# Performance work log

Hardware: AMD Instinct MI355X
Metric: run time of the kernel (lower is better)

## Reference

```python
import jax, jax.numpy as jnp
import numpy as np

SIGMA = 25.0
EPS = 1e-5
TWO_PI = 2.0 * np.pi


def _gn(x, gamma, beta, groups):
    # GroupNorm over (C//G, H, W) per group, per-channel affine.
    B, C, H, W = x.shape
    xg = x.reshape(B, groups, -1)
    m = xg.mean(-1, keepdims=True)
    v = xg.var(-1, keepdims=True)
    xn = ((xg - m) * jax.lax.rsqrt(v + EPS)).reshape(B, C, H, W)
    return xn * gamma[None, :, None, None] + beta[None, :, None, None]


def _conv3(x, k, b):
    y = jax.lax.conv_general_dilated(x, k, (1, 1), 'SAME',
                                     dimension_numbers=('NCHW', 'OIHW', 'NCHW'))
    return y + b[None, :, None, None]


def _tconv2(x, k, b):
    # ConvTranspose2d kernel=2 stride=2 (no overlap) == einsum + reshape.
    # k: [C_in, C_out, 2, 2]
    B, C, H, W = x.shape
    O = k.shape[1]
    y = jnp.einsum('bchw,codq->bohdwq', x, k).reshape(B, O, 2 * H, 2 * W)
    return y + b[None, :, None, None]


def _conv1(x, k, b):
    # 1x1 conv; k: [C_out, C_in]
    return jnp.einsum('bchw,oc->bohw', x, k) + b[None, :, None, None]


def _pool(x):
    B, C, H, W = x.shape
    return x.reshape(B, C, H // 2, 2, W // 2, 2).max(axis=(3, 5))


def _std(t):
    return jnp.sqrt((SIGMA ** (2.0 * t) - 1.0) / (2.0 * jnp.log(SIGMA)))


def setup_inputs() -> dict:
    key = jax.random.key(0)
    ks = jax.random.split(key, 16)
    B, H, W = 64, 128, 128
    E = 2 * W  # 256 = embed_dim

    def w(k, shape, fan_in):
        return jax.random.normal(k, shape, jnp.float32) / np.sqrt(fan_in)

    inp = {
        'x': jax.random.normal(ks[0], (B, 1, H, W), jnp.float32),
        't': jax.random.uniform(ks[1], (B,), jnp.float32, 1e-3, 1.0),
        'Wf': jax.random.normal(ks[2], (H, W), jnp.float32) * 30.0,  # fixed Fourier features
        'fc1_w': w(ks[3], (E, E), E),
        'fc1_b': jnp.zeros((E,), jnp.float32),
        'conv1_k': w(ks[4], (6, 1, 3, 3), 9),
        'conv1_b': jnp.zeros((6,), jnp.float32),
        'gn1_g': jnp.ones((6,), jnp.float32), 'gn1_b': jnp.zeros((6,), jnp.float32),
        'conv2_k': w(ks[5], (24, 6, 3, 3), 6 * 9),
        'conv2_b': jnp.zeros((24,), jnp.float32),
        'gn2_g': jnp.ones((24,), jnp.float32), 'gn2_b': jnp.zeros((24,), jnp.float32),
        't3_k': w(ks[6], (24, 24, 2, 2), 24 * 4),
        't3_b': jnp.zeros((24,), jnp.float32),
        'gn3_g': jnp.ones((48,), jnp.float32), 'gn3_b': jnp.zeros((48,), jnp.float32),
        't4_k': w(ks[7], (48, 12, 2, 2), 48 * 4),
        't4_b': jnp.zeros((12,), jnp.float32),
        'gn4_g': jnp.ones((18,), jnp.float32), 'gn4_b': jnp.zeros((18,), jnp.float32),
        't5_k': w(ks[8], (6, 18), 18),
        't5_b': jnp.zeros((6,), jnp.float32),
        'gn5_g': jnp.ones((6,), jnp.float32), 'gn5_b': jnp.zeros((6,), jnp.float32),
        'fin_k': w(ks[9], (1, 6), 6),
        'fin_b': jnp.zeros((1,), jnp.float32),
    }
    return inp


def reference(x, t, Wf, fc1_w, fc1_b, conv1_k, conv1_b, gn1_g, gn1_b,
              conv2_k, conv2_b, gn2_g, gn2_b, t3_k, t3_b, gn3_g, gn3_b,
              t4_k, t4_b, gn4_g, gn4_b, t5_k, t5_b, gn5_g, gn5_b,
              fin_k, fin_b):
    # Vectorized Gaussian Fourier projection: [B,1,H,W] -> [B,1,H,2W]
    p = x * Wf[None, None] * TWO_PI
    xe = jnp.concatenate([jnp.sin(p), jnp.cos(p)], axis=-1)
    # fc1 on last dim (embed_dim = 2W)
    xf = jnp.einsum('bchw,ow->bcho', xe, fc1_w) + fc1_b
    c1 = _conv3(xf, conv1_k, conv1_b)                              # [B,6,H,2W]
    p1 = _pool(jax.nn.relu(_gn(c1, gn1_g, gn1_b, 6)))              # [B,6,H/2,W]
    c2 = _conv3(p1, conv2_k, conv2_b)                              # [B,24,H/2,W]
    p2 = _pool(jax.nn.relu(_gn(c2, gn2_g, gn2_b, 24)))             # [B,24,H/4,W/2]
    a = p2 * jax.nn.sigmoid(p2)                                    # SiLU bottleneck
    u3 = _tconv2(a, t3_k, t3_b)                                    # [B,24,H/2,W]
    g3 = _gn(jnp.concatenate([c2, u3], axis=1), gn3_g, gn3_b, 6)   # 48 ch
    u4 = _tconv2(g3, t4_k, t4_b)                                   # [B,12,H,2W]
    g4 = _gn(jnp.concatenate([c1, u4], axis=1), gn4_g, gn4_b, 6)   # 18 ch
    u5 = _conv1(g4, t5_k, t5_b)                                    # [B,6,H,2W]
    g5 = _gn(u5, gn5_g, gn5_b, 6)
    return _conv1(g5, fin_k, fin_b) / _std(t)[:, None, None, None]
```

## Files before the change

### kernel.cpp

```cpp
#include <hip/hip_runtime.h>
#include <hip/hip_bf16.h>
#include <math.h>

#define BB 64
#define HH 128
#define WW 128
#define EE 256
#define HP (HH*EE)
#define H2 64
#define W2 128
#define PL2 (H2*W2)
#define H4 32
#define W4 64
#define PL4 (H4*W4)

typedef __hip_bfloat16 bf;
typedef unsigned short ushortt;
typedef __attribute__((ext_vector_type(8))) __bf16 b8v;
typedef __attribute__((ext_vector_type(4))) float f4v;

__device__ __forceinline__ float tof(bf v)    { return __bfloat162float(v); }
__device__ __forceinline__ bf    tob(float v) { return __float2bfloat16(v); }
__device__ __forceinline__ unsigned int bfbits(float v) {
    return (unsigned int)__builtin_bit_cast(ushortt, __float2bfloat16(v));
}
__device__ __forceinline__ float b2f(unsigned int u16) {
    unsigned int x = u16 << 16;
    return __builtin_bit_cast(float, x);
}
__device__ __forceinline__ void wred2(float& s, float& q) {
    #pragma unroll
    for (int m = 32; m; m >>= 1) {
        s += __shfl_xor(s, m);
        q += __shfl_xor(q, m);
    }
}
__device__ __forceinline__ void wred2_32(float& s, float& q) {
    #pragma unroll
    for (int m = 16; m; m >>= 1) {
        s += __shfl_xor(s, m);
        q += __shfl_xor(q, m);
    }
}

__global__ __launch_bounds__(256) void k_fourier_fc1(
    const float* __restrict__ x, const float* __restrict__ Wf,
    const float* __restrict__ fc1_w, const float* __restrict__ fc1_b,
    bf* __restrict__ xf, float* __restrict__ mb)
{
    __shared__ ushortt sA[64*264];
    __shared__ ushortt sB[64*264];
    int t = threadIdx.x;
    for (int i = blockIdx.x*256 + t; i < 9216; i += 512*256) mb[i] = 0.f;
    int rb = blockIdx.x >> 2, cb = blockIdx.x & 3;
    int row0 = rb*64, col0 = cb*64;
    const float TP = 6.2831853071795864769f;
    for (int it = 0; it < 32; ++it) {
        int i = it*256 + t;
        int r = i >> 7, w = i & 127;
        int rg = row0 + r;
        float p = x[(size_t)rg*WW + w] * Wf[(size_t)(rg & (HH-1))*WW + w] * TP;
        sA[r*264 + w]       = (ushortt)bfbits(__sinf(p));
        sA[r*264 + 128 + w] = (ushortt)bfbits(__cosf(p));
    }
    #pragma unroll
    for (int it = 0; it < 16; ++it) {
        int i = it*256 + t;
        int o = i >> 6, c4 = i & 63;
        float4 w4 = *(const float4*)(fc1_w + (size_t)(col0 + o)*EE + c4*4);
        uint2 pk;
        pk.x = bfbits(w4.x) | (bfbits(w4.y) << 16);
        pk.y = bfbits(w4.z) | (bfbits(w4.w) << 16);
        *(uint2*)&sB[o*264 + c4*4] = pk;
    }
    __syncthreads();
    int lane = t & 63, wid = t >> 6;
    int m = lane & 15, kq = (lane >> 4) * 8;
    f4v acc[4] = {};
    const ushortt* aBase = &sA[(wid*16 + m)*264 + kq];
    #pragma unroll
    for (int k0 = 0; k0 < 8; ++k0) {
        b8v av = *(const b8v*)(aBase + k0*32);
        #pragma unroll
        for (int t4 = 0; t4 < 4; ++t4) {
            b8v bv = *(const b8v*)&sB[(t4*16 + m)*264 + k0*32 + kq];
            acc[t4] = __builtin_amdgcn_mfma_f32_16x16x32_bf16(av, bv, acc[t4], 0, 0, 0);
        }
    }
    int rbase = row0 + wid*16 + (lane >> 4)*4;
    #pragma unroll
    for (int t4 = 0; t4 < 4; ++t4) {
        int col = col0 + t4*16 + m;
        float bias = fc1_b[col];
        #pragma unroll
        for (int r = 0; r < 4; ++r)
            xf[(size_t)(rbase + r)*EE + col] = tob(acc[t4][r] + bias);
    }
}

__global__ __launch_bounds__(256) void k_conv1(
    const bf* __restrict__ xf, const float* __restrict__ k,
    const float* __restrict__ bias, bf* __restrict__ c1, float* __restrict__ mc1)
{
    __shared__ ushortt sT[6*272];
    __shared__ float red[4][6][2];
    int t = threadIdx.x;
    int ht = blockIdx.x & 31, b = blockIdx.x >> 5;
    int h0 = ht*4;
    const bf* src = xf + (size_t)b*HP;
    if (t < 192) {
        int r = t >> 5, i = t & 31;
        int gy = h0 - 1 + r;
        uint4 v = {0,0,0,0};
        if (gy >= 0 && gy < HH) v = *(const uint4*)(src + (size_t)gy*EE + i*8);
        *(uint4*)&sT[r*272 + 8 + i*8] = v;
    } else if (t < 204) {
        int e = t - 192;
        int r = e >> 1, s = e & 1;
        uint4 z = {0,0,0,0};
        *(uint4*)&sT[r*272 + s*264] = z;
    }
    __syncthreads();
    int wq = (t & 63)*4, hl = t >> 6;
    int lane = t & 63, wid = t >> 6;
    float v[3][6];
    #pragma unroll
    for (int ky = 0; ky < 3; ++ky)
      #pragma unroll
      for (int j = 0; j < 6; ++j)
        v[ky][j] = b2f((unsigned)sT[(hl+ky)*272 + 7 + wq + j]);
    int h = h0 + hl;
    #pragma unroll
    for (int o = 0; o < 6; ++o) {
        float bv = bias[o];
        float a0=bv, a1=bv, a2=bv, a3=bv;
        #pragma unroll
        for (int ky = 0; ky < 3; ++ky)
          #pragma unroll
          for (int kx = 0; kx < 3; ++kx) {
            float wv = k[o*9 + ky*3 + kx];
            a0 += v[ky][kx+0]*wv;
            a1 += v[ky][kx+1]*wv;
            a2 += v[ky][kx+2]*wv;
            a3 += v[ky][kx+3]*wv;
          }
        uint2 pk;
        pk.x = bfbits(a0) | (bfbits(a1) << 16);
        pk.y = bfbits(a2) | (bfbits(a3) << 16);
        *(uint2*)(c1 + ((size_t)(b*6+o)*HH + h)*EE + wq) = pk;
        float s = a0+a1+a2+a3, q = a0*a0+a1*a1+a2*a2+a3*a3;
        wred2(s, q);
        if (lane == 0) { red[wid][o][0] = s; red[wid][o][1] = q; }
    }
    __syncthreads();
    if (t < 6) {
        float S = 0.f, Q = 0.f;
        #pragma unroll
        for (int wv = 0; wv < 4; ++wv) { S += red[wv][t][0]; Q += red[wv][t][1]; }
        atomicAdd(&mc1[((size_t)b*6 + t)*2],     S);
        atomicAdd(&mc1[((size_t)b*6 + t)*2 + 1], Q);
    }
}

__global__ __launch_bounds__(256) void k_conv2(
    const bf* __restrict__ c1, const float* __restrict__ mc1,
    const float* __restrict__ g1, const float* __restrict__ be1,
    const float* __restrict__ kw, const float* __restrict__ bias,
    bf* __restrict__ c2, float* __restrict__ mc2)
{
    __shared__ ushortt sA[256*72];
    __shared__ ushortt sW[32*72];
    __shared__ ushortt sP[6*4*136];
    __shared__ float ssl[12];
    __shared__ float redS[24], redQ[24];
    int t = threadIdx.x;
    int ht = blockIdx.x & 31, b = blockIdx.x >> 5;
    int h0 = ht*2;
    int lane = t & 63, wid = t >> 6;
    if (t < 24) { redS[t] = 0.f; redQ[t] = 0.f; }
    if (t < 6) {
        float s = mc1[((size_t)b*6 + t)*2], q = mc1[((size_t)b*6 + t)*2 + 1];
        float mean = s * (1.f/HP);
        float var  = q * (1.f/HP) - mean*mean;
        float rstd = rsqrtf(var + 1e-5f);
        float sc = g1[t]*rstd;
        ssl[t*2] = sc; ssl[t*2+1] = be1[t] - mean*sc;
    }
    for (int i = t; i < 1152; i += 256) ((unsigned*)sW)[i] = 0;
    __syncthreads();
    for (int i = t; i < 3120; i += 256) {
        int c = i / 520, rem = i % 520;
        int ry = rem / 130, rx = rem % 130;
        int gy = h0 - 1 + ry, gx = rx - 1;
        float v = 0.f;
        if (gy >= 0 && gy < H2 && gx >= 0 && gx < W2) {
            const bf* pp = c1 + ((size_t)(b*6+c)*HH + 2*gy)*EE + 2*gx;
            unsigned r0 = *(const unsigned*)pp;
            unsigned r1 = *(const unsigned*)(pp + EE);
            float sc = ssl[c*2], sh = ssl[c*2+1];
            float e0 = fmaxf(b2f(r0 & 0xffff)*sc+sh, 0.f);
            float e1 = fmaxf(b2f(r0 >> 16)   *sc+sh, 0.f);
            float e2 = fmaxf(b2f(r1 & 0xffff)*sc+sh, 0.f);
            float e3 = fmaxf(b2f(r1 >> 16)   *sc+sh, 0.f);
            v = fmaxf(fmaxf(e0,e1), fmaxf(e2,e3));
        }
        sP[c*544 + ry*136 + rx] = (ushortt)bfbits(v);
    }
    for (int e = t; e < 1296; e += 256) {
        int o = e / 54, kk = e % 54;
        sW[o*72 + kk] = (ushortt)bfbits(kw[e]);
    }
    __syncthreads();
    {
        int r = t >> 7, xx = t & 127;
        unsigned u[32];
        #pragma unroll
        for (int p = 0; p < 27; ++p) {
            int k0 = 2*p, k1 = 2*p + 1;
            int c0 = k0/9, y0 = (k0%9)/3, x0 = k0%3;
            int c1i = k1/9, y1 = (k1%9)/3, x1 = k1%3;
            unsigned lo = sP[c0*544 + (r+y0)*136 + xx + x0];
            unsigned hi = sP[c1i*544 + (r+y1)*136 + xx + x1];
            u[p] = lo | (hi << 16);
        }
        #pragma unroll
        for (int p = 27; p < 32; ++p) u[p] = 0;
        #pragma unroll
        for (int e = 0; e < 8; ++e) {
            uint4 pk; pk.x = u[4*e]; pk.y = u[4*e+1]; pk.z = u[4*e+2]; pk.w = u[4*e+3];
            *(uint4*)&sA[t*72 + e*8] = pk;
        }
    }
    __syncthreads();
    int m = lane & 15, kq = (lane >> 4)*8;
    b8v wv[2][2];
    #pragma unroll
    for (int nt = 0; nt < 2; ++nt)
      #pragma unroll
      for (int ks = 0; ks < 2; ++ks)
        wv[nt][ks] = *(const b8v*)&sW[(nt*16 + m)*72 + ks*32 + kq];
    f4v acc[4][2] = {};
    #pragma unroll
    for (int mt = 0; mt < 4; ++mt) {
        const ushortt* ab = &sA[(wid*64 + mt*16 + m)*72 + kq];
        b8v a0 = *(const b8v*)(ab);
        b8v a1 = *(const b8v*)(ab + 32);
        #pragma unroll
        for (int nt = 0; nt < 2; ++nt) {
            acc[mt][nt] = __builtin_amdgcn_mfma_f32_16x16x32_bf16(a0, wv[nt][0], acc[mt][nt], 0, 0, 0);
            acc[mt][nt] = __builtin_amdgcn_mfma_f32_16x16x32_bf16(a1, wv[nt][1], acc[mt][nt], 0, 0, 0);
        }
    }
    __syncthreads();
    ushortt* sC = sA;
    int q4 = lane >> 4;
    #pragma unroll
    for (int mt = 0; mt < 4; ++mt) {
        int pxb = wid*64 + mt*16 + q4*4;
        #pragma unroll
        for (int nt = 0; nt < 2; ++nt) {
            int o = nt*16 + m;
            if (o < 24) {
                float bo = bias[o];
                #pragma unroll
                for (int r = 0; r < 4; ++r) {
                    int px = pxb + r;
                    sC[o*272 + (px >> 7)*136 + (px & 127)] =
                        (ushortt)bfbits(acc[mt][nt][r] + bo);
                }
            }
        }
    }
    __syncthreads();
    #pragma unroll
    for (int j = 0; j < 3; ++j) {
        int idx = j*256 + t;
        int o = idx >> 5;
        int rem = idx & 31;
        int r = rem >> 4, x8 = (rem & 15)*8;
        uint4 v = *(const uint4*)&sC[o*272 + r*136 + x8];
        *(uint4*)(c2 + ((size_t)(b*24+o)*H2 + h0 + r)*W2 + x8) = v;
        float v0 = b2f(v.x & 0xffff), v1 = b2f(v.x >> 16);
        float v2 = b2f(v.y & 0xffff), v3 = b2f(v.y >> 16);
        float v4 = b2f(v.z & 0xffff), v5 = b2f(v.z >> 16);
        float v6 = b2f(v.w & 0xffff), v7 = b2f(v.w >> 16);
        float s = v0+v1+v2+v3+v4+v5+v6+v7;
        float qv = v0*v0+v1*v1+v2*v2+v3*v3+v4*v4+v5*v5+v6*v6+v7*v7;
        wred2_32(s, qv);
        if ((lane & 31) == 0) { atomicAdd(&redS[o], s); atomicAdd(&redQ[o], qv); }
    }
    __syncthreads();
    if (t < 24) {
        atomicAdd(&mc2[((size_t)b*24 + t)*2],     redS[t]);
        atomicAdd(&mc2[((size_t)b*24 + t)*2 + 1], redQ[t]);
    }
}

__global__ __launch_bounds__(256) void k_tconv3(
    const bf* __restrict__ c2, const float* __restrict__ mc2,
    const float* __restrict__ g2, const float* __restrict__ be2,
    const float* __restrict__ k3, const float* __restrict__ b3,
    bf* __restrict__ u3, float* __restrict__ mu3)
{
    __shared__ ushortt sBuf[27648];
    __shared__ float redS[24], redQ[24];
    __shared__ float ssl[48];
    ushortt* sA = sBuf;
    ushortt* sW = sBuf + 10240;
    int t = threadIdx.x;
    int b = blockIdx.x >> 3, pg = blockIdx.x & 7;
    int lane = t & 63, wid = t >> 6;
    if (t < 24) {
        redS[t] = 0.f; redQ[t] = 0.f;
        float s = mc2[((size_t)b*24 + t)*2], q = mc2[((size_t)b*24 + t)*2 + 1];
        float mean = s * (1.f/PL2);
        float var  = q * (1.f/PL2) - mean*mean;
        float rstd = rsqrtf(var + 1e-5f);
        float sc = g2[t]*rstd;
        ssl[t*2] = sc; ssl[t*2+1] = be2[t] - mean*sc;
    }
    #pragma unroll
    for (int j = 0; j < 9; ++j) {
        int e = j*256 + t;
        int c = e / 96, n = e % 96;
        sW[n*40 + c] = (ushortt)bfbits(k3[e]);
    }
    if (t < 96) { uint4 z = {0,0,0,0}; *(uint4*)&sW[t*40 + 24] = z; }
    { uint4 z = {0,0,0,0}; *(uint4*)&sA[t*40 + 24] = z; }
    __syncthreads();
    #pragma unroll
    for (int j = 0; j < 12; ++j) {
        int i = j*256 + t;
        int c = i >> 7, pr = i & 127;
        int px0 = pr*2;
        int h4 = (pg*256 + px0) >> 6, w4 = px0 & 63;
        const bf* pp = c2 + ((size_t)b*24 + c)*PL2 + (size_t)(2*h4)*W2 + 2*w4;
        uint2 r0 = *(const uint2*)pp;
        uint2 r1 = *(const uint2*)(pp + W2);
        float sc = ssl[c*2], sh = ssl[c*2+1];
        float e0 = fmaxf(b2f(r0.x & 0xffff)*sc+sh, 0.f);
        float e1 = fmaxf(b2f(r0.x >> 16)   *sc+sh, 0.f);
        float f0 = fmaxf(b2f(r1.x & 0xffff)*sc+sh, 0.f);
        float f1 = fmaxf(b2f(r1.x >> 16)   *sc+sh, 0.f);
        float m0 = fmaxf(fmaxf(e0,e1), fmaxf(f0,f1));
        m0 = m0 / (1.f + expf(-m0));
        float e2 = fmaxf(b2f(r0.y & 0xffff)*sc+sh, 0.f);
        float e3 = fmaxf(b2f(r0.y >> 16)   *sc+sh, 0.f);
        float f2 = fmaxf(b2f(r1.y & 0xffff)*sc+sh, 0.f);
        float f3 = fmaxf(b2f(r1.y >> 16)   *sc+sh, 0.f);
        float m1 = fmaxf(fmaxf(e2,e3), fmaxf(f2,f3));
        m1 = m1 / (1.f + expf(-m1));
        sA[px0*40 + c]     = (ushortt)bfbits(m0);
        sA[(px0+1)*40 + c] = (ushortt)bfbits(m1);
    }
    __syncthreads();
    int m = lane & 15, kq = (lane >> 4)*8;
    b8v wv[6];
    #pragma unroll
    for (int nt = 0; nt < 6; ++nt)
        wv[nt] = *(const b8v*)&sW[(nt*16 + m)*40 + kq];
    f4v acc[4][6] = {};
    #pragma unroll
    for (int mt = 0; mt < 4; ++mt) {
        b8v av = *(const b8v*)&sA[(wid*64 + mt*16 + m)*40 + kq];
        #pragma unroll
        for (int nt = 0; nt < 6; ++nt)
            acc[mt][nt] = __builtin_amdgcn_mfma_f32_16x16x32_bf16(av, wv[nt], acc[mt][nt], 0, 0, 0);
    }
    __syncthreads();
    ushortt* sC = sBuf;
    int q4 = lane >> 4;
    #pragma unroll
    for (int mt = 0; mt < 4; ++mt) {
        int pxb = wid*64 + mt*16 + q4*4;
        #pragma unroll
        for (int nt = 0; nt < 6; ++nt) {
            int n = nt*16 + m;
            int o = n >> 2, d = (n >> 1) & 1, qq = n & 1;
            float bo = b3[o];
            #pragma unroll
            for (int r = 0; r < 4; ++r) {
                int px = pxb + r;
                int yl = ((px >> 6) << 1) + d;
                int xx = ((px & 63) << 1) + qq;
                sC[o*1152 + yl*144 + xx] = (ushortt)bfbits(acc[mt][nt][r] + bo);
            }
        }
    }
    __syncthreads();
    bf* outb = u3 + (size_t)b*24*PL2;
    #pragma unroll
    for (int j = 0; j < 12; ++j) {
        int idx = j*256 + t;
        int o = idx >> 7;
        int rem = idx & 127;
        int yl = rem >> 4, xc = (rem & 15)*8;
        uint4 v = *(const uint4*)&sC[o*1152 + yl*144 + xc];
        *(uint4*)(outb + ((size_t)o*H2 + pg*8 + yl)*W2 + xc) = v;
        float v0 = b2f(v.x & 0xffff), v1 = b2f(v.x >> 16);
        float v2 = b2f(v.y & 0xffff), v3 = b2f(v.y >> 16);
        float v4 = b2f(v.z & 0xffff), v5 = b2f(v.z >> 16);
        float v6 = b2f(v.w & 0xffff), v7 = b2f(v.w >> 16);
        float s = v0+v1+v2+v3+v4+v5+v6+v7;
        float qv = v0*v0+v1*v1+v2*v2+v3*v3+v4*v4+v5*v5+v6*v6+v7*v7;
        wred2(s, qv);
        if (lane == 0) { atomicAdd(&redS[o], s); atomicAdd(&redQ[o], qv); }
    }
    __syncthreads();
    if (t < 24) {
        atomicAdd(&mu3[((size_t)b*24 + t)*2],     redS[t]);
        atomicAdd(&mu3[((size_t)b*24 + t)*2 + 1], redQ[t]);
    }
}

__global__ __launch_bounds__(256) void k_tconv4(
    const bf* __restrict__ c2, const bf* __restrict__ u3,
    const float* __restrict__ mc2, const float* __restrict__ mu3,
    const float* __restrict__ g3, const float* __restrict__ be3,
    const float* __restrict__ k4, const float* __restrict__ bias4,
    bf* __restrict__ u4, float* __restrict__ mu4)
{
    __shared__ ushortt sA[256*64];
    __shared__ ushortt sW[48*64];
    __shared__ float redS[12], redQ[12];
    __shared__ float ssl[96];
    int t = threadIdx.x;
    int b = blockIdx.x >> 5, pg = blockIdx.x & 31;
    int lane = t & 63, wid = t >> 6;
    int m = lane & 15, q4 = lane >> 4;
    if (t < 12) { redS[t] = 0.f; redQ[t] = 0.f; }
    if (t < 6) {
        float s = 0.f, q = 0.f;
        #pragma unroll
        for (int cl = 0; cl < 8; ++cl) {
            int gc = t*8 + cl;
            const float* p = (gc < 24) ? mc2 + ((size_t)b*24 + gc)*2
                                       : mu3 + ((size_t)b*24 + gc - 24)*2;
            s += p[0]; q += p[1];
        }
        float inv_n = 1.f/((float)PL2*8.f);
        float mean = s*inv_n;
        float var  = q*inv_n - mean*mean;
        float rstd = rsqrtf(var + 1e-5f);
        #pragma unroll
        for (int cl = 0; cl < 8; ++cl) {
            int gc = t*8 + cl;
            float sc = g3[gc]*rstd;
            ssl[gc*2] = sc; ssl[gc*2+1] = be3[gc] - mean*sc;
        }
    }
    #pragma unroll
    for (int j = 0; j < 9; ++j) {
        int e = j*256 + t;
        int c = e / 48, n = e % 48;
        sW[n*64 + ((((c >> 3) ^ (n & 7)) << 3) | (c & 7))] = (ushortt)bfbits(k4[e]);
    }
    if (t < 96) {
        uint4 z = {0,0,0,0};
        int n = t >> 1, kb = 6 + (t & 1);
        *(uint4*)&sW[n*64 + ((kb ^ (n & 7)) << 3)] = z;
    }
    {
        int px = t;
        int pix = pg*256 + px;
        const bf* c2p = c2 + (size_t)b*24*PL2 + pix;
        const bf* u3p = u3 + (size_t)b*24*PL2 + pix;
        #pragma unroll
        for (int g = 0; g < 6; ++g) {
            unsigned pr[4];
            #pragma unroll
            for (int hc = 0; hc < 4; ++hc) {
                int c0 = g*8 + hc*2;
                float r0 = (c0 < 24) ? tof(c2p[(size_t)c0*PL2]) : tof(u3p[(size_t)(c0-24)*PL2]);
                float r1 = (c0+1 < 24) ? tof(c2p[(size_t)(c0+1)*PL2]) : tof(u3p[(size_t)(c0+1-24)*PL2]);
                float v0 = r0 * ssl[2*c0]   + ssl[2*c0+1];
                float v1 = r1 * ssl[2*c0+2] + ssl[2*c0+3];
                pr[hc] = bfbits(v0) | (bfbits(v1) << 16);
            }
            uint4 pk; pk.x = pr[0]; pk.y = pr[1]; pk.z = pr[2]; pk.w = pr[3];
            *(uint4*)&sA[px*64 + ((g ^ (px & 7)) << 3)] = pk;
        }
        uint4 z = {0,0,0,0};
        *(uint4*)&sA[px*64 + ((6 ^ (px & 7)) << 3)] = z;
        *(uint4*)&sA[px*64 + ((7 ^ (px & 7)) << 3)] = z;
    }
    __syncthreads();
    b8v bfr[3][2];
    #pragma unroll
    for (int nt = 0; nt < 3; ++nt) {
        int n = nt*16 + m;
        #pragma unroll
        for (int ks = 0; ks < 2; ++ks)
            bfr[nt][ks] = *(const b8v*)&sW[n*64 + (((ks*4 + q4) ^ (n & 7)) << 3)];
    }
    f4v acc[4][3] = {};
    #pragma unroll
    for (int mt = 0; mt < 4; ++mt) {
        int px = wid*64 + mt*16 + m;
        b8v a0 = *(const b8v*)&sA[px*64 + (((q4)     ^ (px & 7)) << 3)];
        b8v a1 = *(const b8v*)&sA[px*64 + (((4 + q4) ^ (px & 7)) << 3)];
        #pragma unroll
        for (int nt = 0; nt < 3; ++nt) {
            acc[mt][nt] = __builtin_amdgcn_mfma_f32_16x16x32_bf16(a0, bfr[nt][0], acc[mt][nt], 0, 0, 0);
            acc[mt][nt] = __builtin_amdgcn_mfma_f32_16x16x32_bf16(a1, bfr[nt][1], acc[mt][nt], 0, 0, 0);
        }
    }
    float sAcc[3] = {0.f, 0.f, 0.f}, qAcc[3] = {0.f, 0.f, 0.f};
    int qq = m & 1;
    #pragma unroll
    for (int nt = 0; nt < 3; ++nt) {
        int n = nt*16 + m;
        int o = n >> 2, d = (n >> 1) & 1;
        float bo = bias4[o];
        #pragma unroll
        for (int mt = 0; mt < 4; ++mt) {
            int pxb = wid*64 + mt*16 + q4*4;
            unsigned wds[4];
            float s = 0.f, q = 0.f;
            #pragma unroll
            for (int r = 0; r < 4; ++r) {
                float v = acc[mt][nt][r] + bo;
                float vp = __shfl_xor(v, 1);
                unsigned lo = bfbits(v), hi = bfbits(vp);
                wds[r] = lo | (hi << 16);
                float f0 = b2f(lo), f1 = b2f(hi);
                s += f0 + f1;
                q += f0*f0 + f1*f1;
            }
            if (qq == 0) {
                int h2 = (pg*256 + pxb) >> 7;
                int w0 = pxb & 127;
                uint4 pk; pk.x = wds[0]; pk.y = wds[1]; pk.z = wds[2]; pk.w = wds[3];
                *(uint4*)(u4 + (((size_t)(b*12 + o))*HH + 2*h2 + d)*EE + 2*w0) = pk;
                sAcc[nt] += s; qAcc[nt] += q;
            }
        }
    }
    #pragma unroll
    for (int nt = 0; nt < 3; ++nt) {
        float s = sAcc[nt], q = qAcc[nt];
        s += __shfl_xor(s, 2);  q += __shfl_xor(q, 2);
        s += __shfl_xor(s, 16); q += __shfl_xor(q, 16);
        s += __shfl_xor(s, 32); q += __shfl_xor(q, 32);
        if ((lane & 51) == 0) {
            int o = nt*4 + (m >> 2);
            atomicAdd(&redS[o], s);
            atomicAdd(&redQ[o], q);
        }
    }
    __syncthreads();
    if (t < 12) {
        atomicAdd(&mu4[((size_t)b*12 + t)*2],     redS[t]);
        atomicAdd(&mu4[((size_t)b*12 + t)*2 + 1], redQ[t]);
    }
}

__global__ __launch_bounds__(256) void k_conv1x1_u5(
    const bf* __restrict__ c1, const bf* __restrict__ u4,
    const float* __restrict__ mc1, const float* __restrict__ mu4,
    const float* __restrict__ g4, const float* __restrict__ be4,
    const float* __restrict__ k, const float* __restrict__ bias,
    bf* __restrict__ u5, float* __restrict__ mu5)
{
    __shared__ float red[4][6][2];
    __shared__ float ssl[36];
    int t = threadIdx.x;
    int b  = blockIdx.x >> 4;
    int pg = blockIdx.x & 15;
    int pix = pg*2048 + t*8;
    int lane = t & 63, wid = t >> 6;
    if (t < 6) {
        float s = 0.f, q = 0.f;
        #pragma unroll
        for (int cl = 0; cl < 3; ++cl) {
            int gc = t*3 + cl;
            const float* p = (gc < 6) ? mc1 + ((size_t)b*6 + gc)*2
                                      : mu4 + ((size_t)b*12 + gc - 6)*2;
            s += p[0]; q += p[1];
        }
        float inv_n = 1.f/((float)HP*3.f);
        float mean = s*inv_n;
        float var  = q*inv_n - mean*mean;
        float rstd = rsqrtf(var + 1e-5f);
        #pragma unroll
        for (int cl = 0; cl < 3; ++cl) {
            int gc = t*3 + cl;
            float sc = g4[gc]*rstd;
            ssl[gc*2] = sc; ssl[gc*2+1] = be4[gc] - mean*sc;
        }
    }
    __syncthreads();
    const bf* c1p = c1 + ((size_t)b*6)*HP + pix;
    const bf* u4p = u4 + ((size_t)b*12)*HP + pix;
    float acc[6][8];
    #pragma unroll
    for (int o = 0; o < 6; ++o) {
        float bv = bias[o];
        #pragma unroll
        for (int j = 0; j < 8; ++j) acc[o][j] = bv;
    }
    #pragma unroll
    for (int c = 0; c < 18; ++c) {
        uint4 r = (c < 6) ? *(const uint4*)(c1p + (size_t)c*HP)
                          : *(const uint4*)(u4p + (size_t)(c-6)*HP);
        float sc = ssl[2*c], sh = ssl[2*c+1];
        float v[8];
        v[0] = b2f(r.x & 0xffff)*sc + sh;  v[1] = b2f(r.x >> 16)*sc + sh;
        v[2] = b2f(r.y & 0xffff)*sc + sh;  v[3] = b2f(r.y >> 16)*sc + sh;
        v[4] = b2f(r.z & 0xffff)*sc + sh;  v[5] = b2f(r.z >> 16)*sc + sh;
        v[6] = b2f(r.w & 0xffff)*sc + sh;  v[7] = b2f(r.w >> 16)*sc + sh;
        #pragma unroll
        for (int o = 0; o < 6; ++o) {
            float wv = k[o*18 + c];
            #pragma unroll
            for (int j = 0; j < 8; ++j) acc[o][j] += v[j]*wv;
        }
    }
    #pragma unroll
    for (int o = 0; o < 6; ++o) {
        uint4 pk;
        pk.x = bfbits(acc[o][0]) | (bfbits(acc[o][1]) << 16);
        pk.y = bfbits(acc[o][2]) | (bfbits(acc[o][3]) << 16);
        pk.z = bfbits(acc[o][4]) | (bfbits(acc[o][5]) << 16);
        pk.w = bfbits(acc[o][6]) | (bfbits(acc[o][7]) << 16);
        *(uint4*)(u5 + ((size_t)(b*6+o))*HP + pix) = pk;
        float s = 0.f, q = 0.f;
        #pragma unroll
        for (int j = 0; j < 8; ++j) { s += acc[o][j]; q += acc[o][j]*acc[o][j]; }
        wred2(s, q);
        if (lane == 0) { red[wid][o][0] = s; red[wid][o][1] = q; }
    }
    __syncthreads();
    if (t < 6) {
        float S = 0.f, Q = 0.f;
        #pragma unroll
        for (int wv = 0; wv < 4; ++wv) { S += red[wv][t][0]; Q += red[wv][t][1]; }
        atomicAdd(&mu5[((size_t)b*6 + t)*2],     S);
        atomicAdd(&mu5[((size_t)b*6 + t)*2 + 1], Q);
    }
}

__global__ __launch_bounds__(256) void k_final(
    const bf* __restrict__ u5, const float* __restrict__ mu5,
    const float* __restrict__ g5, const float* __restrict__ be5,
    const float* __restrict__ k, const float* __restrict__ bias,
    const float* __restrict__ t, float* __restrict__ out)
{
    __shared__ float ssl[12];
    int tt = threadIdx.x;
    int b = blockIdx.x >> 4;
    int pix = ((blockIdx.x & 15)*256 + tt)*8;
    if (tt < 6) {
        float s = mu5[((size_t)b*6 + tt)*2], q = mu5[((size_t)b*6 + tt)*2 + 1];
        float mean = s * (1.f/HP);
        float var  = q * (1.f/HP) - mean*mean;
        float rstd = rsqrtf(var + 1e-5f);
        float sc = g5[tt]*rstd;
        ssl[tt*2] = sc; ssl[tt*2+1] = be5[tt] - mean*sc;
    }
    __syncthreads();
    const bf* up = u5 + (size_t)b*6*HP + pix;
    float bv = bias[0];
    float a[8];
    #pragma unroll
    for (int j = 0; j < 8; ++j) a[j] = bv;
    #pragma unroll
    for (int c = 0; c < 6; ++c) {
        uint4 r = *(const uint4*)(up + (size_t)c*HP);
        float sc = ssl[2*c], sh = ssl[2*c+1];
        float wv = k[c];
        a[0] += (b2f(r.x & 0xffff)*sc + sh) * wv;
        a[1] += (b2f(r.x >> 16)   *sc + sh) * wv;
        a[2] += (b2f(r.y & 0xffff)*sc + sh) * wv;
        a[3] += (b2f(r.y >> 16)   *sc + sh) * wv;
        a[4] += (b2f(r.z & 0xffff)*sc + sh) * wv;
        a[5] += (b2f(r.z >> 16)   *sc + sh) * wv;
        a[6] += (b2f(r.w & 0xffff)*sc + sh) * wv;
        a[7] += (b2f(r.w >> 16)   *sc + sh) * wv;
    }
    float tb = t[b];
    const float lns = 3.2188758248682007492f;
    float var = (expf(2.f*tb*lns) - 1.f) / (2.f*lns);
    float rs = rsqrtf(var);
    float4 o0; o0.x = a[0]*rs; o0.y = a[1]*rs; o0.z = a[2]*rs; o0.w = a[3]*rs;
    float4 o1; o1.x = a[4]*rs; o1.y = a[5]*rs; o1.z = a[6]*rs; o1.w = a[7]*rs;
    float* op = out + (size_t)b*HP + pix;
    *(float4*)op       = o0;
    *(float4*)(op + 4) = o1;
}

extern "C" void kernel_launch(void* const* d_in, const int* in_sizes, int n_in,
                              void* d_out, int out_size, void* d_ws, size_t ws_size,
                              hipStream_t stream)
{
    const float* x       = (const float*)d_in[0];
    const float* t       = (const float*)d_in[1];
    const float* Wf      = (const float*)d_in[2];
    const float* fc1_w   = (const float*)d_in[3];
    const float* fc1_b   = (const float*)d_in[4];
    const float* conv1_k = (const float*)d_in[5];
    const float* conv1_b = (const float*)d_in[6];
    const float* gn1_g   = (const float*)d_in[7];
    const float* gn1_b   = (const float*)d_in[8];
    const float* conv2_k = (const float*)d_in[9];
    const float* conv2_b = (const float*)d_in[10];
    const float* gn2_g   = (const float*)d_in[11];
    const float* gn2_b   = (const float*)d_in[12];
    const float* t3_k    = (const float*)d_in[13];
    const float* t3_b    = (const float*)d_in[14];
    const float* gn3_g   = (const float*)d_in[15];
    const float* gn3_b   = (const float*)d_in[16];
    const float* t4_k    = (const float*)d_in[17];
    const float* t4_b    = (const float*)d_in[18];
    const float* gn4_g   = (const float*)d_in[19];
    const float* gn4_b   = (const float*)d_in[20];
    const float* t5_k    = (const float*)d_in[21];
    const float* t5_b    = (const float*)d_in[22];
    const float* gn5_g   = (const float*)d_in[23];
    const float* gn5_b   = (const float*)d_in[24];
    const float* fin_k   = (const float*)d_in[25];
    const float* fin_b   = (const float*)d_in[26];

    bf* wsb = (bf*)d_ws;
    bf* c1 = wsb;
    bf* c2 = wsb + 12582912;
    bf* u3 = wsb + 25165824;
    bf* u4 = wsb + 37748736;
    bf* xf = wsb + 39845888;
    bf* u5 = wsb + 12582912;
    float* mb = (float*)(wsb + 62914560);
    float* mc1 = mb;
    float* mc2 = mb + 768;
    float* mu3 = mb + 3840;
    float* mu4 = mb + 6912;
    float* mu5 = mb + 8448;

    k_fourier_fc1<<<512, 256, 0, stream>>>(x, Wf, fc1_w, fc1_b, xf, mb);
    k_conv1<<<2048, 256, 0, stream>>>(xf, conv1_k, conv1_b, c1, mc1);
    k_conv2<<<2048, 256, 0, stream>>>(c1, mc1, gn1_g, gn1_b,
                                      conv2_k, conv2_b, c2, mc2);
    k_tconv3<<<512, 256, 0, stream>>>(c2, mc2, gn2_g, gn2_b,
                                      t3_k, t3_b, u3, mu3);
    k_tconv4<<<2048, 256, 0, stream>>>(c2, u3, mc2, mu3, gn3_g, gn3_b,
                                       t4_k, t4_b, u4, mu4);
    k_conv1x1_u5<<<1024, 256, 0, stream>>>(c1, u4, mc1, mu4, gn4_g, gn4_b,
                                           t5_k, t5_b, u5, mu5);
    k_final<<<1024, 256, 0, stream>>>(u5, mu5, gn5_g, gn5_b,
                                      fin_k, fin_b, t, (float*)d_out);
}
```

Before: 236.6 us.

## Swizzle LDS layouts and write conv2/tconv3 outputs directly from MFMA registers

Replaces the padded LDS strides in conv2 and tconv3 with XOR-swizzled 64-element rows, aimed at avoiding bank conflicts without padding. The epilogues no longer stage results through shared memory. Each lane now writes packed bf16 straight to global memory, and GroupNorm partial sums are reduced with shuffles, which drops two barriers and an LDS round trip. tconv3 also gathers eight channels per pixel per thread, so its A-tile stores become 16-byte vectors. The cost is narrower, less coalesced global writes (8- or 16-byte chunks scattered across channels) and more shuffle work.

```diff
diff --git a/kernel.cpp b/kernel.cpp
--- a/kernel.cpp
+++ b/kernel.cpp
@@ -31,13 +31,6 @@
 __device__ __forceinline__ void wred2(float& s, float& q) {
     #pragma unroll
     for (int m = 32; m; m >>= 1) {
-        s += __shfl_xor(s, m);
-        q += __shfl_xor(q, m);
-    }
-}
-__device__ __forceinline__ void wred2_32(float& s, float& q) {
-    #pragma unroll
-    for (int m = 16; m; m >>= 1) {
         s += __shfl_xor(s, m);
         q += __shfl_xor(q, m);
     }
@@ -168,8 +161,8 @@
     const float* __restrict__ kw, const float* __restrict__ bias,
     bf* __restrict__ c2, float* __restrict__ mc2)
 {
-    __shared__ ushortt sA[256*72];
-    __shared__ ushortt sW[32*72];
+    __shared__ ushortt sA[256*64];
+    __shared__ ushortt sW[32*64];
     __shared__ ushortt sP[6*4*136];
     __shared__ float ssl[12];
     __shared__ float redS[24], redQ[24];
@@ -177,6 +170,7 @@
     int ht = blockIdx.x & 31, b = blockIdx.x >> 5;
     int h0 = ht*2;
     int lane = t & 63, wid = t >> 6;
+    int m = lane & 15, q4 = lane >> 4;
     if (t < 24) { redS[t] = 0.f; redQ[t] = 0.f; }
     if (t < 6) {
         float s = mc1[((size_t)b*6 + t)*2], q = mc1[((size_t)b*6 + t)*2 + 1];
@@ -186,7 +180,7 @@
         float sc = g1[t]*rstd;
         ssl[t*2] = sc; ssl[t*2+1] = be1[t] - mean*sc;
     }
-    for (int i = t; i < 1152; i += 256) ((unsigned*)sW)[i] = 0;
+    for (int i = t; i < 1024; i += 256) ((unsigned*)sW)[i] = 0;
     __syncthreads();
     for (int i = t; i < 3120; i += 256) {
         int c = i / 520, rem = i % 520;
@@ -208,7 +202,7 @@
     }
     for (int e = t; e < 1296; e += 256) {
         int o = e / 54, kk = e % 54;
-        sW[o*72 + kk] = (ushortt)bfbits(kw[e]);
+        sW[o*64 + ((((kk >> 3) ^ (o & 7)) << 3) | (kk & 7))] = (ushortt)bfbits(kw[e]);
     }
     __syncthreads();
     {
@@ -228,66 +222,60 @@
         #pragma unroll
         for (int e = 0; e < 8; ++e) {
             uint4 pk; pk.x = u[4*e]; pk.y = u[4*e+1]; pk.z = u[4*e+2]; pk.w = u[4*e+3];
-            *(uint4*)&sA[t*72 + e*8] = pk;
-        }
-    }
-    __syncthreads();
-    int m = lane & 15, kq = (lane >> 4)*8;
+            *(uint4*)&sA[t*64 + ((e ^ (t & 7)) << 3)] = pk;
+        }
+    }
+    __syncthreads();
     b8v wv[2][2];
     #pragma unroll
-    for (int nt = 0; nt < 2; ++nt)
-      #pragma unroll
-      for (int ks = 0; ks < 2; ++ks)
-        wv[nt][ks] = *(const b8v*)&sW[(nt*16 + m)*72 + ks*32 + kq];
+    for (int nt = 0; nt < 2; ++nt) {
+        int o = nt*16 + m;
+        #pragma unroll
+        for (int ks = 0; ks < 2; ++ks)
+            wv[nt][ks] = *(const b8v*)&sW[o*64 + (((ks*4 + q4) ^ (o & 7)) << 3)];
+    }
     f4v acc[4][2] = {};
     #pragma unroll
     for (int mt = 0; mt < 4; ++mt) {
-        const ushortt* ab = &sA[(wid*64 + mt*16 + m)*72 + kq];
-        b8v a0 = *(const b8v*)(ab);
-        b8v a1 = *(const b8v*)(ab + 32);
+        int px = wid*64 + mt*16 + m;
+        b8v a0 = *(const b8v*)&sA[px*64 + (((q4)     ^ (px & 7)) << 3)];
+        b8v a1 = *(const b8v*)&sA[px*64 + (((4 + q4) ^ (px & 7)) << 3)];
         #pragma unroll
         for (int nt = 0; nt < 2; ++nt) {
             acc[mt][nt] = __builtin_amdgcn_mfma_f32_16x16x32_bf16(a0, wv[nt][0], acc[mt][nt], 0, 0, 0);
             acc[mt][nt] = __builtin_amdgcn_mfma_f32_16x16x32_bf16(a1, wv[nt][1], acc[mt][nt], 0, 0, 0);
         }
     }
-    __syncthreads();
-    ushortt* sC = sA;
-    int q4 = lane >> 4;
-    #pragma unroll
-    for (int mt = 0; mt < 4; ++mt) {
-        int pxb = wid*64 + mt*16 + q4*4;
-        #pragma unroll
-        for (int nt = 0; nt < 2; ++nt) {
-            int o = nt*16 + m;
-            if (o < 24) {
-                float bo = bias[o];
-                #pragma unroll
-                for (int r = 0; r < 4; ++r) {
-                    int px = pxb + r;
-                    sC[o*272 + (px >> 7)*136 + (px & 127)] =
-                        (ushortt)bfbits(acc[mt][nt][r] + bo);
-                }
+    float sAcc[2] = {0.f, 0.f}, qAcc[2] = {0.f, 0.f};
+    #pragma unroll
+    for (int nt = 0; nt < 2; ++nt) {
+        int o = nt*16 + m;
+        bool valid = (o < 24);
+        float bo = valid ? bias[o] : 0.f;
+        #pragma unroll
+        for (int mt = 0; mt < 4; ++mt) {
+            int pxb = wid*64 + mt*16 + q4*4;
+            unsigned l0 = bfbits(acc[mt][nt][0] + bo);
+            unsigned l1 = bfbits(acc[mt][nt][1] + bo);
+            unsigned l2 = bfbits(acc[mt][nt][2] + bo);
+            unsigned l3 = bfbits(acc[mt][nt][3] + bo);
+            if (valid) {
+                uint2 pk; pk.x = l0 | (l1 << 16); pk.y = l2 | (l3 << 16);
+                int r = pxb >> 7, xx = pxb & 127;
+                *(uint2*)(c2 + ((size_t)(b*24+o))*PL2 + (size_t)(h0 + r)*W2 + xx) = pk;
+                float f0 = b2f(l0), f1 = b2f(l1), f2 = b2f(l2), f3 = b2f(l3);
+                sAcc[nt] += f0+f1+f2+f3;
+                qAcc[nt] += f0*f0+f1*f1+f2*f2+f3*f3;
             }
         }
     }
-    __syncthreads();
-    #pragma unroll
-    for (int j = 0; j < 3; ++j) {
-        int idx = j*256 + t;
-        int o = idx >> 5;
-        int rem = idx & 31;
-        int r = rem >> 4, x8 = (rem & 15)*8;
-        uint4 v = *(const uint4*)&sC[o*272 + r*136 + x8];
-        *(uint4*)(c2 + ((size_t)(b*24+o)*H2 + h0 + r)*W2 + x8) = v;
-        float v0 = b2f(v.x & 0xffff), v1 = b2f(v.x >> 16);
-        float v2 = b2f(v.y & 0xffff), v3 = b2f(v.y >> 16);
-        float v4 = b2f(v.z & 0xffff), v5 = b2f(v.z >> 16);
-        float v6 = b2f(v.w & 0xffff), v7 = b2f(v.w >> 16);
-        float s = v0+v1+v2+v3+v4+v5+v6+v7;
-        float qv = v0*v0+v1*v1+v2*v2+v3*v3+v4*v4+v5*v5+v6*v6+v7*v7;
-        wred2_32(s, qv);
-        if ((lane & 31) == 0) { atomicAdd(&redS[o], s); atomicAdd(&redQ[o], qv); }
+    #pragma unroll
+    for (int nt = 0; nt < 2; ++nt) {
+        int o = nt*16 + m;
+        float s = sAcc[nt], q = qAcc[nt];
+        s += __shfl_xor(s, 16); q += __shfl_xor(q, 16);
+        s += __shfl_xor(s, 32); q += __shfl_xor(q, 32);
+        if (q4 == 0 && o < 24) { atomicAdd(&redS[o], s); atomicAdd(&redQ[o], q); }
     }
     __syncthreads();
     if (t < 24) {
@@ -302,14 +290,14 @@
     const float* __restrict__ k3, const float* __restrict__ b3,
     bf* __restrict__ u3, float* __restrict__ mu3)
 {
-    __shared__ ushortt sBuf[27648];
+    __shared__ ushortt sA[256*64];
+    __shared__ ushortt sW[96*64];
     __shared__ float redS[24], redQ[24];
     __shared__ float ssl[48];
-    ushortt* sA = sBuf;
-    ushortt* sW = sBuf + 10240;
     int t = threadIdx.x;
     int b = blockIdx.x >> 3, pg = blockIdx.x & 7;
     int lane = t & 63, wid = t >> 6;
+    int m = lane & 15, q4 = lane >> 4;
     if (t < 24) {
         redS[t] = 0.f; redQ[t] = 0.f;
         float s = mc2[((size_t)b*24 + t)*2], q = mc2[((size_t)b*24 + t)*2 + 1];
@@ -319,92 +307,108 @@
         float sc = g2[t]*rstd;
         ssl[t*2] = sc; ssl[t*2+1] = be2[t] - mean*sc;
     }
+    if (t < 96) {
+        uint4 z = {0,0,0,0};
+        *(uint4*)&sW[t*64 + (((3 ^ (t & 3)) + (t & 4)) << 3)] = z;
+    }
     #pragma unroll
     for (int j = 0; j < 9; ++j) {
         int e = j*256 + t;
         int c = e / 96, n = e % 96;
-        sW[n*40 + c] = (ushortt)bfbits(k3[e]);
-    }
-    if (t < 96) { uint4 z = {0,0,0,0}; *(uint4*)&sW[t*40 + 24] = z; }
-    { uint4 z = {0,0,0,0}; *(uint4*)&sA[t*40 + 24] = z; }
-    __syncthreads();
-    #pragma unroll
-    for (int j = 0; j < 12; ++j) {
-        int i = j*256 + t;
-        int c = i >> 7, pr = i & 127;
-        int px0 = pr*2;
-        int h4 = (pg*256 + px0) >> 6, w4 = px0 & 63;
-        const bf* pp = c2 + ((size_t)b*24 + c)*PL2 + (size_t)(2*h4)*W2 + 2*w4;
-        uint2 r0 = *(const uint2*)pp;
-        uint2 r1 = *(const uint2*)(pp + W2);
-        float sc = ssl[c*2], sh = ssl[c*2+1];
-        float e0 = fmaxf(b2f(r0.x & 0xffff)*sc+sh, 0.f);
-        float e1 = fmaxf(b2f(r0.x >> 16)   *sc+sh, 0.f);
-        float f0 = fmaxf(b2f(r1.x & 0xffff)*sc+sh, 0.f);
-        float f1 = fmaxf(b2f(r1.x >> 16)   *sc+sh, 0.f);
-        float m0 = fmaxf(fmaxf(e0,e1), fmaxf(f0,f1));
-        m0 = m0 / (1.f + expf(-m0));
-        float e2 = fmaxf(b2f(r0.y & 0xffff)*sc+sh, 0.f);
-        float e3 = fmaxf(b2f(r0.y >> 16)   *sc+sh, 0.f);
-        float f2 = fmaxf(b2f(r1.y & 0xffff)*sc+sh, 0.f);
-        float f3 = fmaxf(b2f(r1.y >> 16)   *sc+sh, 0.f);
-        float m1 = fmaxf(fmaxf(e2,e3), fmaxf(f2,f3));
-        m1 = m1 / (1.f + expf(-m1));
-        sA[px0*40 + c]     = (ushortt)bfbits(m0);
-        sA[(px0+1)*40 + c] = (ushortt)bfbits(m1);
-    }
-    __syncthreads();
-    int m = lane & 15, kq = (lane >> 4)*8;
+        sW[n*64 + (((((c >> 3) ^ (n & 3)) + (n & 4)) << 3) | (c & 7))] =
+            (ushortt)bfbits(k3[e]);
+    }
+    {
+        int pix = pg*256 + t;
+        int h4 = pix >> 6, w4 = pix & 63;
+        const bf* base = c2 + (size_t)b*24*PL2 + (size_t)(2*h4)*W2 + 2*w4;
+        #pragma unroll
+        for (int g = 0; g < 3; ++g) {
+            unsigned pr[4];
+            #pragma unroll
+            for (int hc = 0; hc < 4; ++hc) {
+                unsigned two[2];
+                #pragma unroll
+                for (int cc = 0; cc < 2; ++cc) {
+                    int c = g*8 + hc*2 + cc;
+                    const bf* pp = base + (size_t)c*PL2;
+                    unsigned r0 = *(const unsigned*)pp;
+                    unsigned r1 = *(const unsigned*)(pp + W2);
+                    float sc = ssl[c*2], sh = ssl[c*2+1];
+                    float e0 = fmaxf(b2f(r0 & 0xffff)*sc+sh, 0.f);
+                    float e1 = fmaxf(b2f(r0 >> 16)   *sc+sh, 0.f);
+                    float e2 = fmaxf(b2f(r1 & 0xffff)*sc+sh, 0.f);
+                    float e3 = fmaxf(b2f(r1 >> 16)   *sc+sh, 0.f);
+                    float mm = fmaxf(fmaxf(e0,e1), fmaxf(e2,e3));
+                    mm = mm / (1.f + expf(-mm));
+                    two[cc] = bfbits(mm);
+                }
+                pr[hc] = two[0] | (two[1] << 16);
+            }
+            uint4 pk; pk.x = pr[0]; pk.y = pr[1]; pk.z = pr[2]; pk.w = pr[3];
+            *(uint4*)&sA[t*64 + (((g ^ (t & 3)) + (t & 4)) << 3)] = pk;
+        }
+        uint4 z = {0,0,0,0};
+        *(uint4*)&sA[t*64 + (((3 ^ (t & 3)) + (t & 4)) << 3)] = z;
+    }
+    __syncthreads();
     b8v wv[6];
     #pragma unroll
-    for (int nt = 0; nt < 6; ++nt)
-        wv[nt] = *(const b8v*)&sW[(nt*16 + m)*40 + kq];
+    for (int nt = 0; nt < 6; ++nt) {
+        int n = nt*16 + m;
+        wv[nt] = *(const b8v*)&sW[n*64 + (((q4 ^ (n & 3)) + (n & 4)) << 3)];
+    }
     f4v acc[4][6] = {};
     #pragma unroll
     for (int mt = 0; mt < 4; ++mt) {
-        b8v av = *(const b8v*)&sA[(wid*64 + mt*16 + m)*40 + kq];
+        int px = wid*64 + mt*16 + m;
+        b8v av = *(const b8v*)&sA[px*64 + (((q4 ^ (px & 3)) + (px & 4)) << 3)];
         #pragma unroll
         for (int nt = 0; nt < 6; ++nt)
             acc[mt][nt] = __builtin_amdgcn_mfma_f32_16x16x32_bf16(av, wv[nt], acc[mt][nt], 0, 0, 0);
     }
-    __syncthreads();
-    ushortt* sC = sBuf;
-    int q4 = lane >> 4;
-    #pragma unroll
-    for (int mt = 0; mt < 4; ++mt) {
-        int pxb = wid*64 + mt*16 + q4*4;
-        #pragma unroll
-        for (int nt = 0; nt < 6; ++nt) {
-            int n = nt*16 + m;
-            int o = n >> 2, d = (n >> 1) & 1, qq = n & 1;
-            float bo = b3[o];
+    float sAcc[6] = {}, qAcc[6] = {};
+    int qq = m & 1;
+    #pragma unroll
+    for (int nt = 0; nt < 6; ++nt) {
+        int n = nt*16 + m;
+        int o = n >> 2, d = (n >> 1) & 1;
+        float bo = b3[o];
+        #pragma unroll
+        for (int mt = 0; mt < 4; ++mt) {
+            int pxb = wid*64 + mt*16 + q4*4;
+            unsigned wds[4];
+            float s = 0.f, q = 0.f;
             #pragma unroll
             for (int r = 0; r < 4; ++r) {
-                int px = pxb + r;
-                int yl = ((px >> 6) << 1) + d;
-                int xx = ((px & 63) << 1) + qq;
-                sC[o*1152 + yl*144 + xx] = (ushortt)bfbits(acc[mt][nt][r] + bo);
+                float v = acc[mt][nt][r] + bo;
+                float vp = __shfl_xor(v, 1);
+                unsigned lo = bfbits(v), hi = bfbits(vp);
+                wds[r] = lo | (hi << 16);
+                float f0 = b2f(lo), f1 = b2f(hi);
+                s += f0 + f1;
+                q += f0*f0 + f1*f1;
             }
-        }
-    }
-    __syncthreads();
-    bf* outb = u3 + (size_t)b*24*PL2;
-    #pragma unroll
-    for (int j = 0; j < 12; ++j) {
-        int idx = j*256 + t;
-        int o = idx >> 7;
-        int rem = idx & 127;
-        int yl = rem >> 4, xc = (rem & 15)*8;
-        uint4 v = *(const uint4*)&sC[o*1152 + yl*144 + xc];
-        *(uint4*)(outb + ((size_t)o*H2 + pg*8 + yl)*W2 + xc) = v;
-        float v0 = b2f(v.x & 0xffff), v1 = b2f(v.x >> 16);
-        float v2 = b2f(v.y & 0xffff), v3 = b2f(v.y >> 16);
-        float v4 = b2f(v.z & 0xffff), v5 = b2f(v.z >> 16);
-        float v6 = b2f(v.w & 0xffff), v7 = b2f(v.w >> 16);
-        float s = v0+v1+v2+v3+v4+v5+v6+v7;
-        float qv = v0*v0+v1*v1+v2*v2+v3*v3+v4*v4+v5*v5+v6*v6+v7*v7;
-        wred2(s, qv);
-        if (lane == 0) { atomicAdd(&redS[o], s); atomicAdd(&redQ[o], qv); }
+            if (qq == 0) {
+                int h4 = (pg*256 + pxb) >> 6;
+                int w4 = pxb & 63;
+                uint4 pk; pk.x = wds[0]; pk.y = wds[1]; pk.z = wds[2]; pk.w = wds[3];
+                *(uint4*)(u3 + ((size_t)(b*24 + o))*PL2 + (size_t)(2*h4 + d)*W2 + 2*w4) = pk;
+                sAcc[nt] += s; qAcc[nt] += q;
+            }
+        }
+    }
+    #pragma unroll
+    for (int nt = 0; nt < 6; ++nt) {
+        float s = sAcc[nt], q = qAcc[nt];
+        s += __shfl_xor(s, 2);  q += __shfl_xor(q, 2);
+        s += __shfl_xor(s, 16); q += __shfl_xor(q, 16);
+        s += __shfl_xor(s, 32); q += __shfl_xor(q, 32);
+        if ((lane & 51) == 0) {
+            int o = nt*4 + (m >> 2);
+            atomicAdd(&redS[o], s);
+            atomicAdd(&redQ[o], q);
+        }
     }
     __syncthreads();
     if (t < 24) {
```

New measurement: 233.8 us. About the same (-1.2%).
